# Performance work log

Measured on AMD Instinct MI355X. Metric: run time of the kernel, lower is better.

Reference implementation:

```python
import jax, jax.numpy as jnp
import numpy as np

LEAKY_SLOPE = 0.01
BN_EPS = 1e-5


def _local_conv(x, w, b, stride):
    # x: [B,C,H,W]; w: [1,O,C,OH,OW,K] (K = kh*kw, kh==kw); b: [1,O,OH,OW]
    sh, sw = stride
    _, O, C, oh, ow, K = w.shape
    k = int(round(K ** 0.5))
    # gather unfold patches: torch .unfold(2,kh,dh).unfold(3,kw,dw) -> last dim ordered (i major, j minor)
    patches = jnp.stack(
        [x[:, :, i:i + sh * oh:sh, j:j + sw * ow:sw] for i in range(k) for j in range(k)],
        axis=-1)  # [B,C,oh,ow,K]
    out = jnp.einsum('bchwk,ochwk->bohw', patches, w[0])
    return out + b  # b broadcasts [1,O,OH,OW]


def _bn_train(x, gamma, beta):
    # BatchNorm2d in training mode: biased batch statistics over (N,H,W)
    m = jnp.mean(x, axis=(0, 2, 3), keepdims=True)
    v = jnp.var(x, axis=(0, 2, 3), keepdims=True)
    return gamma[None, :, None, None] * (x - m) * jax.lax.rsqrt(v + BN_EPS) + beta[None, :, None, None]


def _lrelu(x):
    return jnp.where(x >= 0, x, LEAKY_SLOPE * x)


def _pad1(x):
    return jnp.pad(x, ((0, 0), (0, 0), (1, 1), (1, 1)))


def setup_inputs() -> dict:
    key = jax.random.key(0)
    ks = jax.random.split(key, 16)
    B = 8192
    inp = {
        'image': jax.random.normal(ks[0], (B, 10, 9, 1), jnp.float32),
        'conv1_w': jax.random.normal(ks[1], (64, 1, 2, 2), jnp.float32) * 0.5,
        'conv1_b': jax.random.normal(ks[2], (64,), jnp.float32) * 0.1,
        'lc1_w': jax.random.normal(ks[3], (1, 16, 64, 10, 5, 9), jnp.float32) * 0.05,
        'lc1_b': jax.random.normal(ks[4], (1, 16, 10, 5), jnp.float32) * 0.1,
        'lc2_w': jax.random.normal(ks[5], (1, 8, 16, 11, 6, 4), jnp.float32) * 0.1,
        'lc2_b': jax.random.normal(ks[6], (1, 8, 11, 6), jnp.float32) * 0.1,
        'lc3_w': jax.random.normal(ks[7], (1, 8, 8, 12, 4, 4), jnp.float32) * 0.1,
        'lc3_b': jax.random.normal(ks[8], (1, 8, 12, 4), jnp.float32) * 0.1,
        'gamma1': jax.random.normal(ks[9], (16,), jnp.float32) * 0.1 + 1.0,
        'beta1': jax.random.normal(ks[10], (16,), jnp.float32) * 0.1,
        'gamma2': jax.random.normal(ks[11], (8,), jnp.float32) * 0.1 + 1.0,
        'beta2': jax.random.normal(ks[12], (8,), jnp.float32) * 0.1,
        'gamma3': jax.random.normal(ks[13], (8,), jnp.float32) * 0.1 + 1.0,
        'beta3': jax.random.normal(ks[14], (8,), jnp.float32) * 0.1,
    }
    return inp


def reference(image, conv1_w, conv1_b, lc1_w, lc1_b, lc2_w, lc2_b, lc3_w, lc3_b,
              gamma1, beta1, gamma2, beta2, gamma3, beta3):
    x = jnp.transpose(image, (0, 3, 1, 2))  # [B,1,10,9]
    # Conv2d kernel 2, padding='same' (torch pads extra on right/bottom for even kernels)
    x = jax.lax.conv_general_dilated(
        x, conv1_w, window_strides=(1, 1), padding=[(0, 1), (0, 1)],
        dimension_numbers=('NCHW', 'OIHW', 'NCHW'))
    x = x + conv1_b[None, :, None, None]
    x = _lrelu(x)
    x = _pad1(x)                               # [B,64,12,11]
    x = _local_conv(x, lc1_w, lc1_b, (1, 2))   # [B,16,10,5]
    x = _lrelu(x)
    x = _bn_train(x, gamma1, beta1)
    x = _pad1(x)                               # [B,16,12,7]
    x = _local_conv(x, lc2_w, lc2_b, (1, 1))   # [B,8,11,6]
    x = _lrelu(x)
    x = _bn_train(x, gamma2, beta2)
    x = _pad1(x)                               # [B,8,13,8]
    x = _local_conv(x, lc3_w, lc3_b, (1, 2))   # [B,8,12,4]
    x = _lrelu(x)
    x = _bn_train(x, gamma3, beta3)
    return x.reshape(x.shape[0], -1)           # [B,384]
```

## Files before the change

### kernel.cpp

```cpp
#include <hip/hip_runtime.h>


#define LR(x) ((x) >= 0.0f ? (x) : 0.01f * (x))

typedef float f32x4 __attribute__((ext_vector_type(4)));
typedef short bf16x8 __attribute__((ext_vector_type(8)));

union FR { int4 i4; bf16x8 bf; unsigned u[4]; };

static __device__ inline unsigned pk2(float hi, float lo) {
    return __builtin_amdgcn_perm(__float_as_uint(hi), __float_as_uint(lo), 0x07060302u);
}
static __device__ inline unsigned bfr(float f) {
    unsigned u = __float_as_uint(f);
    return (u + 0x7fffu + ((u >> 16) & 1u)) >> 16;
}

__global__ __launch_bounds__(64) void k0_zero(float* __restrict__ stats) {
    stats[threadIdx.x] = 0.0f;
}

__global__ __launch_bounds__(256) void kB_wfrag(
    const float* __restrict__ lw,
    int4* __restrict__ afg)
{
    const int pos = blockIdx.x;
    const int tid = threadIdx.x;
    for (int e = tid; e < 1152; e += 256) {
        int l = e & 63, ht = e >> 6;
        int h = ht / 9, t = ht - 9 * h;
        int q = l >> 4, o = l & 15;
        unsigned uu[4];
        #pragma unroll
        for (int jj = 0; jj < 4; ++jj) {
            int c0 = 32 * h + 8 * q + 2 * jj;
            float w0 = lw[(o * 64 + c0) * 450 + pos * 9 + t];
            float w1 = lw[(o * 64 + c0 + 1) * 450 + pos * 9 + t];
            uu[jj] = bfr(w0) | (bfr(w1) << 16);
        }
        int4 st = { (int)uu[0], (int)uu[1], (int)uu[2], (int)uu[3] };
        afg[pos * 1152 + e] = st;
    }
}

__global__ __launch_bounds__(256) void k1_lc1(
    const float* __restrict__ img,
    const float* __restrict__ cw,
    const float* __restrict__ cb,
    const int4* __restrict__ afg,
    const float* __restrict__ lb,
    float* __restrict__ y1,
    float* __restrict__ stats)
{
    __shared__ int4   AfL[1152];
    __shared__ float4 cw4s[64];
    __shared__ float  cbl[64];
    __shared__ float  bl[16];
    __shared__ float  red[32];

    const int pos = blockIdx.x;
    const int oh = pos / 5, ow = pos % 5;
    const int tid = threadIdx.x;
    const int wv = tid >> 6, lane = tid & 63;
    const int lane15 = lane & 15, q = lane >> 4;

    for (int e = tid; e < 1152; e += 256) AfL[e] = afg[pos * 1152 + e];
    if (tid < 64) { cw4s[tid] = ((const float4*)cw)[tid]; cbl[tid] = cb[tid]; }
    if (tid < 16) bl[tid] = lb[tid * 50 + pos];
    if (tid < 32) red[tid] = 0.0f;
    __syncthreads();

    bool km[9];
    #pragma unroll
    for (int i = 0; i < 3; i++)
        #pragma unroll
        for (int j = 0; j < 3; j++) {
            int r = oh + i - 1, c2 = 2 * ow + j - 1;
            km[i * 3 + j] = (r >= 0 && r < 10 && c2 >= 0 && c2 < 9);
        }

    const int sBase = blockIdx.y * 256 + wv * 64;
    float ip[4][16];
    #pragma unroll
    for (int g = 0; g < 4; ++g) {
        const float* ib = img + (size_t)(sBase + g * 16 + lane15) * 90;
        #pragma unroll
        for (int a = 0; a < 4; ++a) {
            int r = oh - 1 + a;
            bool rok = (r >= 0 && r < 10);
            #pragma unroll
            for (int d = 0; d < 4; ++d) {
                int c2 = 2 * ow - 1 + d;
                bool ok = rok && (c2 >= 0 && c2 < 9);
                ip[g][a * 4 + d] = ok ? ib[r * 9 + c2] : 0.0f;
            }
        }
    }

    f32x4 acc[4];
    #pragma unroll
    for (int g = 0; g < 4; ++g) acc[g] = (f32x4){0.f, 0.f, 0.f, 0.f};

    #pragma unroll
    for (int h = 0; h < 2; ++h) {
        float4 wcr[8]; float cbr[8];
        #pragma unroll
        for (int cc = 0; cc < 8; ++cc) {
            wcr[cc] = cw4s[h * 32 + q * 8 + cc];
            cbr[cc] = cbl[h * 32 + q * 8 + cc];
        }
        #pragma unroll
        for (int t = 0; t < 9; ++t) {
            const int ti = t / 3, tj = t % 3;
            const int i0 = ti * 4 + tj;
            if (km[t]) {
                FR fa; fa.i4 = AfL[(h * 9 + t) * 64 + lane];
                #pragma unroll
                for (int g = 0; g < 4; ++g) {
                    float p[8];
                    #pragma unroll
                    for (int cc = 0; cc < 8; ++cc) {
                        float4 wc = wcr[cc];
                        float v = cbr[cc];
                        v = fmaf(ip[g][i0],     wc.x, v);
                        v = fmaf(ip[g][i0 + 1], wc.y, v);
                        v = fmaf(ip[g][i0 + 4], wc.z, v);
                        v = fmaf(ip[g][i0 + 5], wc.w, v);
                        p[cc] = fmaxf(v, 0.01f * v);
                    }
                    FR fb;
                    fb.u[0] = pk2(p[1], p[0]);
                    fb.u[1] = pk2(p[3], p[2]);
                    fb.u[2] = pk2(p[5], p[4]);
                    fb.u[3] = pk2(p[7], p[6]);
                    acc[g] = __builtin_amdgcn_mfma_f32_16x16x32_bf16(fa.bf, fb.bf, acc[g], 0, 0, 0);
                }
            }
        }
    }

    float so[4], sq[4];
    #pragma unroll
    for (int r = 0; r < 4; ++r) { so[r] = 0.f; sq[r] = 0.f; }
    #pragma unroll
    for (int g = 0; g < 4; ++g) {
        #pragma unroll
        for (int r = 0; r < 4; ++r) {
            int o = q * 4 + r;
            float v = acc[g][r] + bl[o];
            v = fmaxf(v, 0.01f * v);
            y1[(size_t)(o * 50 + pos) * 8192 + sBase + g * 16 + lane15] = v;
            so[r] += v; sq[r] += v * v;
        }
    }
    #pragma unroll
    for (int r = 0; r < 4; ++r) {
        #pragma unroll
        for (int m = 1; m < 16; m <<= 1) {
            so[r] += __shfl_xor(so[r], m, 16);
            sq[r] += __shfl_xor(sq[r], m, 16);
        }
        if (lane15 == 0) {
            int o = q * 4 + r;
            atomicAdd(&red[o], so[r]);
            atomicAdd(&red[16 + o], sq[r]);
        }
    }
    __syncthreads();
    if (tid < 32) atomicAdd(&stats[tid], red[tid]);
}

__global__ __launch_bounds__(256) void k2_lc2(
    const float* __restrict__ y1,
    const float* __restrict__ lw,
    const float* __restrict__ lb,
    const float* __restrict__ g1, const float* __restrict__ be1,
    float* __restrict__ y2,
    float* __restrict__ stats)
{
    __shared__ float4 wldv[128];
    __shared__ float a1[16], b1[16];
    __shared__ float bl[8];
    __shared__ float red[16];
    float* wld = (float*)wldv;

    const int pos = blockIdx.x;
    const int oh = pos / 6, ow = pos % 6;
    const int tid = threadIdx.x;

    if (tid < 128) {
        const float* src = lw + tid * 264 + pos * 4;
        int o = tid >> 4, c = tid & 15;
        #pragma unroll
        for (int k = 0; k < 4; k++) wld[c * 32 + k * 8 + o] = src[k];
    }
    if (tid < 16) {
        float m = stats[tid] * (1.0f / 409600.0f);
        float v = stats[16 + tid] * (1.0f / 409600.0f) - m * m;
        float a = g1[tid] * rsqrtf(v + 1e-5f);
        a1[tid] = a; b1[tid] = be1[tid] - a * m;
    }
    if (tid < 8) bl[tid] = lb[tid * 66 + pos];
    if (tid < 16) red[tid] = 0.0f;
    __syncthreads();

    float km[4];
    #pragma unroll
    for (int i = 0; i < 2; i++)
        #pragma unroll
        for (int j = 0; j < 2; j++) {
            int r = oh + i - 1, c2 = ow + j - 1;
            km[i * 2 + j] = (r >= 0 && r < 10 && c2 >= 0 && c2 < 5) ? 1.0f : 0.0f;
        }

    const int sb = blockIdx.y * 1024 + tid;

    float acc[8][4];
    #pragma unroll
    for (int o = 0; o < 8; o++)
        #pragma unroll
        for (int s = 0; s < 4; s++) acc[o][s] = bl[o];

    #pragma unroll 1
    for (int c = 0; c < 16; c++) {
        float a = a1[c], bb = b1[c];
        float p[4][4];
        #pragma unroll
        for (int i = 0; i < 2; i++)
            #pragma unroll
            for (int j = 0; j < 2; j++) {
                int r = oh + i - 1;  r = r < 0 ? 0 : (r > 9 ? 9 : r);
                int c2 = ow + j - 1; c2 = c2 < 0 ? 0 : (c2 > 4 ? 4 : c2);
                const float* src = y1 + (size_t)(c * 50 + r * 5 + c2) * 8192 + sb;
                float kmv = km[i * 2 + j];
                #pragma unroll
                for (int s = 0; s < 4; s++)
                    p[i * 2 + j][s] = kmv * fmaf(a, src[s * 256], bb);
            }
        const float4* wr = wldv + c * 8;
        #pragma unroll
        for (int k = 0; k < 4; k++) {
            float4 wa = wr[k * 2], wb = wr[k * 2 + 1];
            #pragma unroll
            for (int s = 0; s < 4; s++) {
                float pv = p[k][s];
                acc[0][s] += wa.x * pv; acc[1][s] += wa.y * pv;
                acc[2][s] += wa.z * pv; acc[3][s] += wa.w * pv;
                acc[4][s] += wb.x * pv; acc[5][s] += wb.y * pv;
                acc[6][s] += wb.z * pv; acc[7][s] += wb.w * pv;
            }
        }
    }

    #pragma unroll
    for (int o = 0; o < 8; o++) {
        float sv = 0.f, sqv = 0.f;
        float* dst = y2 + (size_t)(o * 66 + pos) * 8192 + sb;
        #pragma unroll
        for (int s = 0; s < 4; s++) {
            float v = LR(acc[o][s]);
            dst[s * 256] = v;
            sv += v; sqv += v * v;
        }
        #pragma unroll
        for (int m = 32; m > 0; m >>= 1) {
            sv  += __shfl_xor(sv, m, 64);
            sqv += __shfl_xor(sqv, m, 64);
        }
        if ((tid & 63) == 0) { atomicAdd(&red[o], sv); atomicAdd(&red[8 + o], sqv); }
    }
    __syncthreads();
    if (tid < 16) atomicAdd(&stats[32 + tid], red[tid]);
}

__global__ __launch_bounds__(256) void k3_lc3(
    const float* __restrict__ y2,
    const float* __restrict__ lw,
    const float* __restrict__ lb,
    const float* __restrict__ g2, const float* __restrict__ be2,
    float* __restrict__ y3,
    float* __restrict__ stats)
{
    __shared__ float4 wldv[64];
    __shared__ float a2[8], b2[8];
    __shared__ float bl[8];
    __shared__ float red[16];
    float* wld = (float*)wldv;

    const int pos = blockIdx.x;
    const int oh = pos >> 2, ow = pos & 3;
    const int tid = threadIdx.x;

    if (tid < 64) {
        const float* src = lw + tid * 192 + pos * 4;
        int o = tid >> 3, c = tid & 7;
        #pragma unroll
        for (int k = 0; k < 4; k++) wld[c * 32 + k * 8 + o] = src[k];
    }
    if (tid < 8) {
        float m = stats[32 + tid] * (1.0f / 540672.0f);
        float v = stats[40 + tid] * (1.0f / 540672.0f) - m * m;
        float a = g2[tid] * rsqrtf(v + 1e-5f);
        a2[tid] = a; b2[tid] = be2[tid] - a * m;
    }
    if (tid < 8) bl[tid] = lb[tid * 48 + pos];
    if (tid < 16) red[tid] = 0.0f;
    __syncthreads();

    float km[4];
    #pragma unroll
    for (int i = 0; i < 2; i++)
        #pragma unroll
        for (int j = 0; j < 2; j++) {
            int r = oh + i - 1, c2 = 2 * ow + j - 1;
            km[i * 2 + j] = (r >= 0 && r < 11 && c2 >= 0 && c2 < 6) ? 1.0f : 0.0f;
        }

    const int sb = blockIdx.y * 1024 + tid;

    float acc[8][4];
    #pragma unroll
    for (int o = 0; o < 8; o++)
        #pragma unroll
        for (int s = 0; s < 4; s++) acc[o][s] = bl[o];

    #pragma unroll 1
    for (int c = 0; c < 8; c++) {
        float a = a2[c], bb = b2[c];
        float p[4][4];
        #pragma unroll
        for (int i = 0; i < 2; i++)
            #pragma unroll
            for (int j = 0; j < 2; j++) {
                int r = oh + i - 1;      r = r < 0 ? 0 : (r > 10 ? 10 : r);
                int c2 = 2 * ow + j - 1; c2 = c2 < 0 ? 0 : (c2 > 5 ? 5 : c2);
                const float* src = y2 + (size_t)(c * 66 + r * 6 + c2) * 8192 + sb;
                float kmv = km[i * 2 + j];
                #pragma unroll
                for (int s = 0; s < 4; s++)
                    p[i * 2 + j][s] = kmv * fmaf(a, src[s * 256], bb);
            }
        const float4* wr = wldv + c * 8;
        #pragma unroll
        for (int k = 0; k < 4; k++) {
            float4 wa = wr[k * 2], wb = wr[k * 2 + 1];
            #pragma unroll
            for (int s = 0; s < 4; s++) {
                float pv = p[k][s];
                acc[0][s] += wa.x * pv; acc[1][s] += wa.y * pv;
                acc[2][s] += wa.z * pv; acc[3][s] += wa.w * pv;
                acc[4][s] += wb.x * pv; acc[5][s] += wb.y * pv;
                acc[6][s] += wb.z * pv; acc[7][s] += wb.w * pv;
            }
        }
    }

    #pragma unroll
    for (int o = 0; o < 8; o++) {
        float sv = 0.f, sqv = 0.f;
        float* dst = y3 + (size_t)(o * 48 + pos) * 8192 + sb;
        #pragma unroll
        for (int s = 0; s < 4; s++) {
            float v = LR(acc[o][s]);
            dst[s * 256] = v;
            sv += v; sqv += v * v;
        }
        #pragma unroll
        for (int m = 32; m > 0; m >>= 1) {
            sv  += __shfl_xor(sv, m, 64);
            sqv += __shfl_xor(sqv, m, 64);
        }
        if ((tid & 63) == 0) { atomicAdd(&red[o], sv); atomicAdd(&red[8 + o], sqv); }
    }
    __syncthreads();
    if (tid < 16) atomicAdd(&stats[48 + tid], red[tid]);
}

__global__ __launch_bounds__(256) void k4_out(
    const float* __restrict__ y3,
    const float* __restrict__ g3, const float* __restrict__ be3,
    const float* __restrict__ stats,
    float* __restrict__ out)
{
    __shared__ float tile[64][65];
    __shared__ float a3[8], b3[8];
    const int tid = threadIdx.x;
    if (tid < 8) {
        float m = stats[48 + tid] * (1.0f / 393216.0f);
        float v = stats[56 + tid] * (1.0f / 393216.0f) - m * m;
        float a = g3[tid] * rsqrtf(v + 1e-5f);
        a3[tid] = a; b3[tid] = be3[tid] - a * m;
    }
    __syncthreads();

    const int fbase = blockIdx.x * 64;
    const int sbase = blockIdx.y * 64;

    #pragma unroll
    for (int rep = 0; rep < 16; rep++) {
        int idx = rep * 256 + tid;
        int f = idx >> 6, s = idx & 63;
        int ff = fbase + f;
        int o = ff / 48;
        float v = y3[(size_t)ff * 8192 + sbase + s];
        tile[f][s] = a3[o] * v + b3[o];
    }
    __syncthreads();
    #pragma unroll
    for (int rep = 0; rep < 16; rep++) {
        int idx = rep * 256 + tid;
        int s = idx >> 6, f = idx & 63;
        out[(size_t)(sbase + s) * 384 + fbase + f] = tile[f][s];
    }
}

extern "C" void kernel_launch(void* const* d_in, const int* in_sizes, int n_in,
                              void* d_out, int out_size, void* d_ws, size_t ws_size,
                              hipStream_t stream) {
    const float* image   = (const float*)d_in[0];
    const float* conv1_w = (const float*)d_in[1];
    const float* conv1_b = (const float*)d_in[2];
    const float* lc1_w   = (const float*)d_in[3];
    const float* lc1_b   = (const float*)d_in[4];
    const float* lc2_w   = (const float*)d_in[5];
    const float* lc2_b   = (const float*)d_in[6];
    const float* lc3_w   = (const float*)d_in[7];
    const float* lc3_b   = (const float*)d_in[8];
    const float* gamma1  = (const float*)d_in[9];
    const float* beta1   = (const float*)d_in[10];
    const float* gamma2  = (const float*)d_in[11];
    const float* beta2   = (const float*)d_in[12];
    const float* gamma3  = (const float*)d_in[13];
    const float* beta3   = (const float*)d_in[14];

    float* ws    = (float*)d_ws;
    float* stats = ws;
    float* y2    = ws + 64;
    float* y1    = ws + 64 + 4325376;
    float* y3    = y1;
    int4*  afg   = (int4*)(ws + 64 + 4325376 + 6553600);

    k0_zero <<<dim3(1),       dim3(64),  0, stream>>>(stats);
    kB_wfrag<<<dim3(50),      dim3(256), 0, stream>>>(lc1_w, afg);
    k1_lc1  <<<dim3(50, 32),  dim3(256), 0, stream>>>(image, conv1_w, conv1_b,
                                                      afg, lc1_b, y1, stats);
    k2_lc2  <<<dim3(66, 8),   dim3(256), 0, stream>>>(y1, lc2_w, lc2_b,
                                                      gamma1, beta1, y2, stats);
    k3_lc3  <<<dim3(48, 8),   dim3(256), 0, stream>>>(y2, lc3_w, lc3_b,
                                                      gamma2, beta2, y3, stats);
    k4_out  <<<dim3(6, 128),  dim3(256), 0, stream>>>(y3, gamma3, beta3, stats,
                                                      (float*)d_out);
}
```

Before: 193.0 us.

## Store intermediates in bf16, move lc2/lc3 to MFMA, merge weight prep kernels

Intermediate activations y1, y2 and y3 are now stored as bf16 rather than fp32, which halves the memory traffic between stages. The lc2 and lc3 local convolutions move from scalar FMA loops to bf16 MFMA using weight fragments prepared ahead of time. The stats zeroing and the three weight-fragment preparations are folded into one kernel, and grid dimensions are swapped so that consecutive blocks walk through samples. The conv1 preactivation uses packed fp32 FMAs. The trade-off is lower precision in intermediates and BN statistics, and half-empty MFMA tiles because O=8 is padded to 16.

```diff
diff --git a/kernel.cpp b/kernel.cpp
--- a/kernel.cpp
+++ b/kernel.cpp
@@ -1,12 +1,14 @@
 #include <hip/hip_runtime.h>
 
 
-#define LR(x) ((x) >= 0.0f ? (x) : 0.01f * (x))
-
-typedef float f32x4 __attribute__((ext_vector_type(4)));
-typedef short bf16x8 __attribute__((ext_vector_type(8)));
-
-union FR { int4 i4; bf16x8 bf; unsigned u[4]; };
+typedef float  f32x4 __attribute__((ext_vector_type(4)));
+typedef float  f32x2 __attribute__((ext_vector_type(2)));
+typedef short  bf16x8 __attribute__((ext_vector_type(8)));
+
+union FR  { int4 i4; bf16x8 bf; unsigned u[4]; };
+union F2U { f32x2 v; unsigned u[2]; float f[2]; };
+
+#define LRELU(v) fmaxf((v), 0.01f * (v))
 
 static __device__ inline unsigned pk2(float hi, float lo) {
     return __builtin_amdgcn_perm(__float_as_uint(hi), __float_as_uint(lo), 0x07060302u);
@@ -15,31 +17,95 @@
     unsigned u = __float_as_uint(f);
     return (u + 0x7fffu + ((u >> 16) & 1u)) >> 16;
 }
-
-__global__ __launch_bounds__(64) void k0_zero(float* __restrict__ stats) {
-    stats[threadIdx.x] = 0.0f;
-}
-
-__global__ __launch_bounds__(256) void kB_wfrag(
-    const float* __restrict__ lw,
-    int4* __restrict__ afg)
+static __device__ inline unsigned short bfr16(float f) { return (unsigned short)bfr(f); }
+
+#if __has_builtin(__builtin_elementwise_fma)
+static __device__ inline f32x2 pk_fma(f32x2 a, f32x2 b, f32x2 c) { return __builtin_elementwise_fma(a, b, c); }
+#else
+static __device__ inline f32x2 pk_fma(f32x2 a, f32x2 b, f32x2 c) { return a * b + c; }
+#endif
+static __device__ inline f32x2 pk_lrelu(f32x2 v) {
+#if __has_builtin(__builtin_elementwise_max)
+    return __builtin_elementwise_max(v, v * 0.01f);
+#else
+    f32x2 r; r.x = LRELU(v.x); r.y = LRELU(v.y); return r;
+#endif
+}
+
+__global__ __launch_bounds__(256) void kB_frags(
+    const float* __restrict__ lw1,
+    const float* __restrict__ lw2,
+    const float* __restrict__ lw3,
+    int4* __restrict__ afg1, int4* __restrict__ afg2, int4* __restrict__ afg3,
+    float* __restrict__ stats)
 {
-    const int pos = blockIdx.x;
-    const int tid = threadIdx.x;
-    for (int e = tid; e < 1152; e += 256) {
-        int l = e & 63, ht = e >> 6;
-        int h = ht / 9, t = ht - 9 * h;
-        int q = l >> 4, o = l & 15;
-        unsigned uu[4];
-        #pragma unroll
-        for (int jj = 0; jj < 4; ++jj) {
-            int c0 = 32 * h + 8 * q + 2 * jj;
-            float w0 = lw[(o * 64 + c0) * 450 + pos * 9 + t];
-            float w1 = lw[(o * 64 + c0 + 1) * 450 + pos * 9 + t];
-            uu[jj] = bfr(w0) | (bfr(w1) << 16);
-        }
-        int4 st = { (int)uu[0], (int)uu[1], (int)uu[2], (int)uu[3] };
-        afg[pos * 1152 + e] = st;
+    const int bx = blockIdx.x, tid = threadIdx.x;
+    if (bx == 0 && tid < 64) stats[tid] = 0.0f;
+
+    if (bx < 50) {
+        const int pos = bx;
+        __shared__ float wt[9216];
+        for (int e = tid; e < 9216; e += 256) {
+            int pair = e / 9, t = e - 9 * pair;
+            wt[e] = lw1[pair * 450 + pos * 9 + t];
+        }
+        __syncthreads();
+        for (int e = tid; e < 1152; e += 256) {
+            int l = e & 63, ht = e >> 6;
+            int h = ht / 9, t = ht - 9 * h;
+            int q = l >> 4, o = l & 15;
+            unsigned uu[4];
+            #pragma unroll
+            for (int p = 0; p < 4; ++p) {
+                int c0 = 32 * h + 8 * q + 2 * p;
+                float w0 = wt[(o * 64 + c0) * 9 + t];
+                float w1 = wt[(o * 64 + c0 + 1) * 9 + t];
+                uu[p] = bfr(w0) | (bfr(w1) << 16);
+            }
+            int4 st = { (int)uu[0], (int)uu[1], (int)uu[2], (int)uu[3] };
+            afg1[pos * 1152 + e] = st;
+        }
+    } else if (bx < 116) {
+        const int pos = bx - 50;
+        if (tid < 128) {
+            int l = tid & 63, h = tid >> 6;
+            int q = l >> 4, o = l & 15;
+            unsigned uu[4];
+            #pragma unroll
+            for (int p = 0; p < 4; ++p) {
+                unsigned w01[2];
+                #pragma unroll
+                for (int d = 0; d < 2; ++d) {
+                    int kg = h * 32 + q * 8 + 2 * p + d;
+                    int c = kg >> 2, t = kg & 3;
+                    float w = (o < 8) ? lw2[(o * 16 + c) * 264 + pos * 4 + t] : 0.0f;
+                    w01[d] = bfr(w);
+                }
+                uu[p] = w01[0] | (w01[1] << 16);
+            }
+            int4 st = { (int)uu[0], (int)uu[1], (int)uu[2], (int)uu[3] };
+            afg2[(pos * 2 + h) * 64 + l] = st;
+        }
+    } else {
+        const int pos = bx - 116;
+        if (tid < 64) {
+            int l = tid, q = l >> 4, o = l & 15;
+            unsigned uu[4];
+            #pragma unroll
+            for (int p = 0; p < 4; ++p) {
+                unsigned w01[2];
+                #pragma unroll
+                for (int d = 0; d < 2; ++d) {
+                    int kg = q * 8 + 2 * p + d;
+                    int c = kg >> 2, t = kg & 3;
+                    float w = (o < 8) ? lw3[(o * 8 + c) * 192 + pos * 4 + t] : 0.0f;
+                    w01[d] = bfr(w);
+                }
+                uu[p] = w01[0] | (w01[1] << 16);
+            }
+            int4 st = { (int)uu[0], (int)uu[1], (int)uu[2], (int)uu[3] };
+            afg3[pos * 64 + l] = st;
+        }
     }
 }
 
@@ -49,7 +115,7 @@
     const float* __restrict__ cb,
     const int4* __restrict__ afg,
     const float* __restrict__ lb,
-    float* __restrict__ y1,
+    unsigned short* __restrict__ y1b,
     float* __restrict__ stats)
 {
     __shared__ int4   AfL[1152];
@@ -58,7 +124,7 @@
     __shared__ float  bl[16];
     __shared__ float  red[32];
 
-    const int pos = blockIdx.x;
+    const int pos = blockIdx.y;
     const int oh = pos / 5, ow = pos % 5;
     const int tid = threadIdx.x;
     const int wv = tid >> 6, lane = tid & 63;
@@ -79,7 +145,7 @@
             km[i * 3 + j] = (r >= 0 && r < 10 && c2 >= 0 && c2 < 9);
         }
 
-    const int sBase = blockIdx.y * 256 + wv * 64;
+    const int sBase = blockIdx.x * 256 + wv * 64;
     float ip[4][16];
     #pragma unroll
     for (int g = 0; g < 4; ++g) {
@@ -103,11 +169,16 @@
 
     #pragma unroll
     for (int h = 0; h < 2; ++h) {
-        float4 wcr[8]; float cbr[8];
-        #pragma unroll
-        for (int cc = 0; cc < 8; ++cc) {
-            wcr[cc] = cw4s[h * 32 + q * 8 + cc];
-            cbr[cc] = cbl[h * 32 + q * 8 + cc];
+        f32x2 wx2[4], wy2[4], wz2[4], ww2[4], cb2[4];
+        #pragma unroll
+        for (int p = 0; p < 4; ++p) {
+            float4 wa = cw4s[h * 32 + q * 8 + 2 * p];
+            float4 wb = cw4s[h * 32 + q * 8 + 2 * p + 1];
+            wx2[p] = (f32x2){wa.x, wb.x};
+            wy2[p] = (f32x2){wa.y, wb.y};
+            wz2[p] = (f32x2){wa.z, wb.z};
+            ww2[p] = (f32x2){wa.w, wb.w};
+            cb2[p] = (f32x2){cbl[h * 32 + q * 8 + 2 * p], cbl[h * 32 + q * 8 + 2 * p + 1]};
         }
         #pragma unroll
         for (int t = 0; t < 9; ++t) {
@@ -117,22 +188,21 @@
                 FR fa; fa.i4 = AfL[(h * 9 + t) * 64 + lane];
                 #pragma unroll
                 for (int g = 0; g < 4; ++g) {
-                    float p[8];
+                    f32x2 s0 = (f32x2)ip[g][i0];
+                    f32x2 s1 = (f32x2)ip[g][i0 + 1];
+                    f32x2 s2 = (f32x2)ip[g][i0 + 4];
+                    f32x2 s3 = (f32x2)ip[g][i0 + 5];
+                    FR fb;
                     #pragma unroll
-                    for (int cc = 0; cc < 8; ++cc) {
-                        float4 wc = wcr[cc];
-                        float v = cbr[cc];
-                        v = fmaf(ip[g][i0],     wc.x, v);
-                        v = fmaf(ip[g][i0 + 1], wc.y, v);
-                        v = fmaf(ip[g][i0 + 4], wc.z, v);
-                        v = fmaf(ip[g][i0 + 5], wc.w, v);
-                        p[cc] = fmaxf(v, 0.01f * v);
+                    for (int p = 0; p < 4; ++p) {
+                        f32x2 v = pk_fma(s0, wx2[p], cb2[p]);
+                        v = pk_fma(s1, wy2[p], v);
+                        v = pk_fma(s2, wz2[p], v);
+                        v = pk_fma(s3, ww2[p], v);
+                        v = pk_lrelu(v);
+                        F2U u; u.v = v;
+                        fb.u[p] = __builtin_amdgcn_perm(u.u[1], u.u[0], 0x07060302u);
                     }
-                    FR fb;
-                    fb.u[0] = pk2(p[1], p[0]);
-                    fb.u[1] = pk2(p[3], p[2]);
-                    fb.u[2] = pk2(p[5], p[4]);
-                    fb.u[3] = pk2(p[7], p[6]);
                     acc[g] = __builtin_amdgcn_mfma_f32_16x16x32_bf16(fa.bf, fb.bf, acc[g], 0, 0, 0);
                 }
             }
@@ -148,8 +218,8 @@
         for (int r = 0; r < 4; ++r) {
             int o = q * 4 + r;
             float v = acc[g][r] + bl[o];
-            v = fmaxf(v, 0.01f * v);
-            y1[(size_t)(o * 50 + pos) * 8192 + sBase + g * 16 + lane15] = v;
+            v = LRELU(v);
+            y1b[(size_t)(o * 50 + pos) * 8192 + sBase + g * 16 + lane15] = bfr16(v);
             so[r] += v; sq[r] += v * v;
         }
     }
@@ -171,213 +241,208 @@
 }
 
 __global__ __launch_bounds__(256) void k2_lc2(
-    const float* __restrict__ y1,
-    const float* __restrict__ lw,
+    const unsigned short* __restrict__ y1b,
+    const int4* __restrict__ afg2,
     const float* __restrict__ lb,
     const float* __restrict__ g1, const float* __restrict__ be1,
-    float* __restrict__ y2,
+    unsigned short* __restrict__ y2b,
     float* __restrict__ stats)
 {
-    __shared__ float4 wldv[128];
-    __shared__ float a1[16], b1[16];
-    __shared__ float bl[8];
+    __shared__ float a1L[16], b1L[16];
+    __shared__ float blL[16];
     __shared__ float red[16];
-    float* wld = (float*)wldv;
-
-    const int pos = blockIdx.x;
+
+    const int pos = blockIdx.y;
     const int oh = pos / 6, ow = pos % 6;
     const int tid = threadIdx.x;
-
-    if (tid < 128) {
-        const float* src = lw + tid * 264 + pos * 4;
-        int o = tid >> 4, c = tid & 15;
-        #pragma unroll
-        for (int k = 0; k < 4; k++) wld[c * 32 + k * 8 + o] = src[k];
-    }
+    const int wv = tid >> 6, lane = tid & 63;
+    const int lane15 = lane & 15, q = lane >> 4;
+
     if (tid < 16) {
         float m = stats[tid] * (1.0f / 409600.0f);
         float v = stats[16 + tid] * (1.0f / 409600.0f) - m * m;
         float a = g1[tid] * rsqrtf(v + 1e-5f);
-        a1[tid] = a; b1[tid] = be1[tid] - a * m;
-    }
-    if (tid < 8) bl[tid] = lb[tid * 66 + pos];
-    if (tid < 16) red[tid] = 0.0f;
-    __syncthreads();
-
-    float km[4];
-    #pragma unroll
-    for (int i = 0; i < 2; i++)
-        #pragma unroll
-        for (int j = 0; j < 2; j++) {
-            int r = oh + i - 1, c2 = ow + j - 1;
-            km[i * 2 + j] = (r >= 0 && r < 10 && c2 >= 0 && c2 < 5) ? 1.0f : 0.0f;
-        }
-
-    const int sb = blockIdx.y * 1024 + tid;
-
-    float acc[8][4];
-    #pragma unroll
-    for (int o = 0; o < 8; o++)
-        #pragma unroll
-        for (int s = 0; s < 4; s++) acc[o][s] = bl[o];
-
-    #pragma unroll 1
-    for (int c = 0; c < 16; c++) {
-        float a = a1[c], bb = b1[c];
-        float p[4][4];
-        #pragma unroll
-        for (int i = 0; i < 2; i++)
+        a1L[tid] = a; b1L[tid] = be1[tid] - a * m;
+        blL[tid] = (tid < 8) ? lb[tid * 66 + pos] : 0.0f;
+        red[tid] = 0.0f;
+    }
+    FR fa[2];
+    fa[0].i4 = afg2[(pos * 2 + 0) * 64 + lane];
+    fa[1].i4 = afg2[(pos * 2 + 1) * 64 + lane];
+    __syncthreads();
+
+    float aa[2][8], bb[2][8];
+    unsigned off[2][8];
+    #pragma unroll
+    for (int h = 0; h < 2; ++h)
+        #pragma unroll
+        for (int j = 0; j < 8; ++j) {
+            int kg = h * 32 + q * 8 + j;
+            int c = kg >> 2, t = kg & 3;
+            int r = oh + (t >> 1) - 1, c2 = ow + (t & 1) - 1;
+            bool ok = (r >= 0 && r < 10 && c2 >= 0 && c2 < 5);
+            int rc = min(max(r, 0), 9), cc2 = min(max(c2, 0), 4);
+            off[h][j] = (unsigned)((c * 50 + rc * 5 + cc2) * 8192);
+            aa[h][j] = ok ? a1L[c] : 0.0f;
+            bb[h][j] = ok ? b1L[c] : 0.0f;
+        }
+
+    const int sWave = blockIdx.x * 256 + wv * 64;
+    f32x4 acc[4];
+    #pragma unroll
+    for (int g = 0; g < 4; ++g) acc[g] = (f32x4){0.f, 0.f, 0.f, 0.f};
+
+    #pragma unroll
+    for (int g = 0; g < 4; ++g) {
+        const unsigned samp = (unsigned)(sWave + g * 16 + lane15);
+        #pragma unroll
+        for (int h = 0; h < 2; ++h) {
+            FR fb;
             #pragma unroll
-            for (int j = 0; j < 2; j++) {
-                int r = oh + i - 1;  r = r < 0 ? 0 : (r > 9 ? 9 : r);
-                int c2 = ow + j - 1; c2 = c2 < 0 ? 0 : (c2 > 4 ? 4 : c2);
-                const float* src = y1 + (size_t)(c * 50 + r * 5 + c2) * 8192 + sb;
-                float kmv = km[i * 2 + j];
-                #pragma unroll
-                for (int s = 0; s < 4; s++)
-                    p[i * 2 + j][s] = kmv * fmaf(a, src[s * 256], bb);
+            for (int p = 0; p < 4; ++p) {
+                int j0 = 2 * p, j1 = 2 * p + 1;
+                float x0 = __uint_as_float((unsigned)y1b[off[h][j0] + samp] << 16);
+                float x1 = __uint_as_float((unsigned)y1b[off[h][j1] + samp] << 16);
+                float p0 = fmaf(aa[h][j0], x0, bb[h][j0]);
+                float p1 = fmaf(aa[h][j1], x1, bb[h][j1]);
+                fb.u[p] = pk2(p1, p0);
             }
-        const float4* wr = wldv + c * 8;
-        #pragma unroll
-        for (int k = 0; k < 4; k++) {
-            float4 wa = wr[k * 2], wb = wr[k * 2 + 1];
-            #pragma unroll
-            for (int s = 0; s < 4; s++) {
-                float pv = p[k][s];
-                acc[0][s] += wa.x * pv; acc[1][s] += wa.y * pv;
-                acc[2][s] += wa.z * pv; acc[3][s] += wa.w * pv;
-                acc[4][s] += wb.x * pv; acc[5][s] += wb.y * pv;
-                acc[6][s] += wb.z * pv; acc[7][s] += wb.w * pv;
-            }
-        }
-    }
-
-    #pragma unroll
-    for (int o = 0; o < 8; o++) {
-        float sv = 0.f, sqv = 0.f;
-        float* dst = y2 + (size_t)(o * 66 + pos) * 8192 + sb;
-        #pragma unroll
-        for (int s = 0; s < 4; s++) {
-            float v = LR(acc[o][s]);
-            dst[s * 256] = v;
-            sv += v; sqv += v * v;
-        }
-        #pragma unroll
-        for (int m = 32; m > 0; m >>= 1) {
-            sv  += __shfl_xor(sv, m, 64);
-            sqv += __shfl_xor(sqv, m, 64);
-        }
-        if ((tid & 63) == 0) { atomicAdd(&red[o], sv); atomicAdd(&red[8 + o], sqv); }
+            acc[g] = __builtin_amdgcn_mfma_f32_16x16x32_bf16(fa[h].bf, fb.bf, acc[g], 0, 0, 0);
+        }
+    }
+
+    float so[4], sq[4];
+    #pragma unroll
+    for (int r = 0; r < 4; ++r) { so[r] = 0.f; sq[r] = 0.f; }
+    #pragma unroll
+    for (int g = 0; g < 4; ++g) {
+        #pragma unroll
+        for (int r = 0; r < 4; ++r) {
+            int row = q * 4 + r;
+            float v = acc[g][r] + blL[row & 15];
+            v = LRELU(v);
+            if (lane < 32)
+                y2b[(size_t)(row * 66 + pos) * 8192 + sWave + g * 16 + lane15] = bfr16(v);
+            so[r] += v; sq[r] += v * v;
+        }
+    }
+    #pragma unroll
+    for (int r = 0; r < 4; ++r) {
+        #pragma unroll
+        for (int m = 1; m < 16; m <<= 1) {
+            so[r] += __shfl_xor(so[r], m, 16);
+            sq[r] += __shfl_xor(sq[r], m, 16);
+        }
+        if (lane15 == 0 && lane < 32) {
+            int row = q * 4 + r;
+            atomicAdd(&red[row], so[r]);
+            atomicAdd(&red[8 + row], sq[r]);
+        }
     }
     __syncthreads();
     if (tid < 16) atomicAdd(&stats[32 + tid], red[tid]);
 }
 
 __global__ __launch_bounds__(256) void k3_lc3(
-    const float* __restrict__ y2,
-    const float* __restrict__ lw,
+    const unsigned short* __restrict__ y2b,
+    const int4* __restrict__ afg3,
     const float* __restrict__ lb,
     const float* __restrict__ g2, const float* __restrict__ be2,
-    float* __restrict__ y3,
+    unsigned short* __restrict__ y3b,
     float* __restrict__ stats)
 {
-    __shared__ float4 wldv[64];
-    __shared__ float a2[8], b2[8];
-    __shared__ float bl[8];
+    __shared__ float a2L[8], b2L[8];
+    __shared__ float blL[16];
     __shared__ float red[16];
-    float* wld = (float*)wldv;
-
-    const int pos = blockIdx.x;
+
+    const int pos = blockIdx.y;
     const int oh = pos >> 2, ow = pos & 3;
     const int tid = threadIdx.x;
-
-    if (tid < 64) {
-        const float* src = lw + tid * 192 + pos * 4;
-        int o = tid >> 3, c = tid & 7;
-        #pragma unroll
-        for (int k = 0; k < 4; k++) wld[c * 32 + k * 8 + o] = src[k];
-    }
-    if (tid < 8) {
-        float m = stats[32 + tid] * (1.0f / 540672.0f);
-        float v = stats[40 + tid] * (1.0f / 540672.0f) - m * m;
-        float a = g2[tid] * rsqrtf(v + 1e-5f);
-        a2[tid] = a; b2[tid] = be2[tid] - a * m;
-    }
-    if (tid < 8) bl[tid] = lb[tid * 48 + pos];
-    if (tid < 16) red[tid] = 0.0f;
-    __syncthreads();
-
-    float km[4];
-    #pragma unroll
-    for (int i = 0; i < 2; i++)
-        #pragma unroll
-        for (int j = 0; j < 2; j++) {
-            int r = oh + i - 1, c2 = 2 * ow + j - 1;
-            km[i * 2 + j] = (r >= 0 && r < 11 && c2 >= 0 && c2 < 6) ? 1.0f : 0.0f;
-        }
-
-    const int sb = blockIdx.y * 1024 + tid;
-
-    float acc[8][4];
-    #pragma unroll
-    for (int o = 0; o < 8; o++)
-        #pragma unroll
-        for (int s = 0; s < 4; s++) acc[o][s] = bl[o];
-
-    #pragma unroll 1
-    for (int c = 0; c < 8; c++) {
-        float a = a2[c], bb = b2[c];
-        float p[4][4];
-        #pragma unroll
-        for (int i = 0; i < 2; i++)
-            #pragma unroll
-            for (int j = 0; j < 2; j++) {
-                int r = oh + i - 1;      r = r < 0 ? 0 : (r > 10 ? 10 : r);
-                int c2 = 2 * ow + j - 1; c2 = c2 < 0 ? 0 : (c2 > 5 ? 5 : c2);
-                const float* src = y2 + (size_t)(c * 66 + r * 6 + c2) * 8192 + sb;
-                float kmv = km[i * 2 + j];
-                #pragma unroll
-                for (int s = 0; s < 4; s++)
-                    p[i * 2 + j][s] = kmv * fmaf(a, src[s * 256], bb);
-            }
-        const float4* wr = wldv + c * 8;
-        #pragma unroll
-        for (int k = 0; k < 4; k++) {
-            float4 wa = wr[k * 2], wb = wr[k * 2 + 1];
-            #pragma unroll
-            for (int s = 0; s < 4; s++) {
-                float pv = p[k][s];
-                acc[0][s] += wa.x * pv; acc[1][s] += wa.y * pv;
-                acc[2][s] += wa.z * pv; acc[3][s] += wa.w * pv;
-                acc[4][s] += wb.x * pv; acc[5][s] += wb.y * pv;
-                acc[6][s] += wb.z * pv; acc[7][s] += wb.w * pv;
-            }
-        }
-    }
-
-    #pragma unroll
-    for (int o = 0; o < 8; o++) {
-        float sv = 0.f, sqv = 0.f;
-        float* dst = y3 + (size_t)(o * 48 + pos) * 8192 + sb;
-        #pragma unroll
-        for (int s = 0; s < 4; s++) {
-            float v = LR(acc[o][s]);
-            dst[s * 256] = v;
-            sv += v; sqv += v * v;
-        }
-        #pragma unroll
-        for (int m = 32; m > 0; m >>= 1) {
-            sv  += __shfl_xor(sv, m, 64);
-            sqv += __shfl_xor(sqv, m, 64);
-        }
-        if ((tid & 63) == 0) { atomicAdd(&red[o], sv); atomicAdd(&red[8 + o], sqv); }
+    const int wv = tid >> 6, lane = tid & 63;
+    const int lane15 = lane & 15, q = lane >> 4;
+
+    if (tid < 16) {
+        if (tid < 8) {
+            float m = stats[32 + tid] * (1.0f / 540672.0f);
+            float v = stats[40 + tid] * (1.0f / 540672.0f) - m * m;
+            float a = g2[tid] * rsqrtf(v + 1e-5f);
+            a2L[tid] = a; b2L[tid] = be2[tid] - a * m;
+        }
+        blL[tid] = (tid < 8) ? lb[tid * 48 + pos] : 0.0f;
+        red[tid] = 0.0f;
+    }
+    FR fa; fa.i4 = afg3[pos * 64 + lane];
+    __syncthreads();
+
+    float aa[8], bb[8];
+    unsigned off[8];
+    #pragma unroll
+    for (int j = 0; j < 8; ++j) {
+        int kg = q * 8 + j;
+        int c = kg >> 2, t = kg & 3;
+        int r = oh + (t >> 1) - 1, c2 = 2 * ow + (t & 1) - 1;
+        bool ok = (r >= 0 && r < 11 && c2 >= 0 && c2 < 6);
+        int rc = min(max(r, 0), 10), cc2 = min(max(c2, 0), 5);
+        off[j] = (unsigned)((c * 66 + rc * 6 + cc2) * 8192);
+        aa[j] = ok ? a2L[c] : 0.0f;
+        bb[j] = ok ? b2L[c] : 0.0f;
+    }
+
+    const int sWave = blockIdx.x * 256 + wv * 64;
+    f32x4 acc[4];
+    #pragma unroll
+    for (int g = 0; g < 4; ++g) acc[g] = (f32x4){0.f, 0.f, 0.f, 0.f};
+
+    #pragma unroll
+    for (int g = 0; g < 4; ++g) {
+        const unsigned samp = (unsigned)(sWave + g * 16 + lane15);
+        FR fb;
+        #pragma unroll
+        for (int p = 0; p < 4; ++p) {
+            int j0 = 2 * p, j1 = 2 * p + 1;
+            float x0 = __uint_as_float((unsigned)y2b[off[j0] + samp] << 16);
+            float x1 = __uint_as_float((unsigned)y2b[off[j1] + samp] << 16);
+            float p0 = fmaf(aa[j0], x0, bb[j0]);
+            float p1 = fmaf(aa[j1], x1, bb[j1]);
+            fb.u[p] = pk2(p1, p0);
+        }
+        acc[g] = __builtin_amdgcn_mfma_f32_16x16x32_bf16(fa.bf, fb.bf, acc[g], 0, 0, 0);
+    }
+
+    float so[4], sq[4];
+    #pragma unroll
+    for (int r = 0; r < 4; ++r) { so[r] = 0.f; sq[r] = 0.f; }
+    #pragma unroll
+    for (int g = 0; g < 4; ++g) {
+        #pragma unroll
+        for (int r = 0; r < 4; ++r) {
+            int row = q * 4 + r;
+            float v = acc[g][r] + blL[row & 15];
+            v = LRELU(v);
+            if (lane < 32)
+                y3b[(size_t)(row * 48 + pos) * 8192 + sWave + g * 16 + lane15] = bfr16(v);
+            so[r] += v; sq[r] += v * v;
+        }
+    }
+    #pragma unroll
+    for (int r = 0; r < 4; ++r) {
+        #pragma unroll
+        for (int m = 1; m < 16; m <<= 1) {
+            so[r] += __shfl_xor(so[r], m, 16);
+            sq[r] += __shfl_xor(sq[r], m, 16);
+        }
+        if (lane15 == 0 && lane < 32) {
+            int row = q * 4 + r;
+            atomicAdd(&red[row], so[r]);
+            atomicAdd(&red[8 + row], sq[r]);
+        }
     }
     __syncthreads();
     if (tid < 16) atomicAdd(&stats[48 + tid], red[tid]);
 }
 
 __global__ __launch_bounds__(256) void k4_out(
-    const float* __restrict__ y3,
+    const unsigned short* __restrict__ y3b,
     const float* __restrict__ g3, const float* __restrict__ be3,
     const float* __restrict__ stats,
     float* __restrict__ out)
@@ -393,8 +458,9 @@
     }
     __syncthreads();
 
-    const int fbase = blockIdx.x * 64;
-    const int sbase = blockIdx.y * 64;
+    const int ftile = blockIdx.y >> 2, sub = blockIdx.y & 3;
+    const int fbase = ftile * 64;
+    const int sbase = blockIdx.x * 256 + sub * 64;
 
     #pragma unroll
     for (int rep = 0; rep < 16; rep++) {
@@ -402,8 +468,8 @@
         int f = idx >> 6, s = idx & 63;
         int ff = fbase + f;
         int o = ff / 48;
-        float v = y3[(size_t)ff * 8192 + sbase + s];
-        tile[f][s] = a3[o] * v + b3[o];
+        float x = __uint_as_float((unsigned)y3b[(size_t)ff * 8192 + sbase + s] << 16);
+        tile[f][s] = a3[o] * x + b3[o];
     }
     __syncthreads();
     #pragma unroll
@@ -433,21 +499,23 @@
     const float* gamma3  = (const float*)d_in[13];
     const float* beta3   = (const float*)d_in[14];
 
-    float* ws    = (float*)d_ws;
-    float* stats = ws;
-    float* y2    = ws + 64;
-    float* y1    = ws + 64 + 4325376;
-    float* y3    = y1;
-    int4*  afg   = (int4*)(ws + 64 + 4325376 + 6553600);
-
-    k0_zero <<<dim3(1),       dim3(64),  0, stream>>>(stats);
-    kB_wfrag<<<dim3(50),      dim3(256), 0, stream>>>(lc1_w, afg);
-    k1_lc1  <<<dim3(50, 32),  dim3(256), 0, stream>>>(image, conv1_w, conv1_b,
-                                                      afg, lc1_b, y1, stats);
-    k2_lc2  <<<dim3(66, 8),   dim3(256), 0, stream>>>(y1, lc2_w, lc2_b,
-                                                      gamma1, beta1, y2, stats);
-    k3_lc3  <<<dim3(48, 8),   dim3(256), 0, stream>>>(y2, lc3_w, lc3_b,
-                                                      gamma2, beta2, y3, stats);
-    k4_out  <<<dim3(6, 128),  dim3(256), 0, stream>>>(y3, gamma3, beta3, stats,
+    char* wsb = (char*)d_ws;
+    float*          stats = (float*)wsb;
+    unsigned short* y1b   = (unsigned short*)(wsb + 1024);
+    unsigned short* y2b   = (unsigned short*)(wsb + 13108224);
+    unsigned short* y3b   = (unsigned short*)(wsb + 21758976);
+    int4*           afg1  = (int4*)(wsb + 28050432);
+    int4*           afg2  = (int4*)(wsb + 28972032);
+    int4*           afg3  = (int4*)(wsb + 29107200);
+
+    kB_frags<<<dim3(164),     dim3(256), 0, stream>>>(lc1_w, lc2_w, lc3_w,
+                                                      afg1, afg2, afg3, stats);
+    k1_lc1  <<<dim3(32, 50),  dim3(256), 0, stream>>>(image, conv1_w, conv1_b,
+                                                      afg1, lc1_b, y1b, stats);
+    k2_lc2  <<<dim3(32, 66),  dim3(256), 0, stream>>>(y1b, afg2, lc2_b,
+                                                      gamma1, beta1, y2b, stats);
+    k3_lc3  <<<dim3(32, 48),  dim3(256), 0, stream>>>(y2b, afg3, lc3_b,
+                                                      gamma2, beta2, y3b, stats);
+    k4_out  <<<dim3(32, 24),  dim3(256), 0, stream>>>(y3b, gamma3, beta3, stats,
                                                       (float*)d_out);
 }
```

After: 215.9 us. 11.9% more time.
